# Optimization experiments

Hardware: AMD Instinct MI355X
Metric: run time of the kernel (lower is better)

Reference implementation:

```python
import jax, jax.numpy as jnp
import numpy as np

T = 65536  # number of frames

# Precomputed strict upper-triangle index pairs (matches htriu/ptriu/ltriu masks:
# dist+1 >= 1 > 0 everywhere, so boolean_mask((dist+1)*triu != 0) followed by -1
# is exactly 'take dist at strict upper-triangle entries').
_HIU = np.triu_indices(21, k=1)  # 210 pairs
_PIU = np.triu_indices(25, k=1)  # 300 pairs
_LIU = np.triu_indices(20, k=1)  # 190 pairs


def _triu_dist(pts, iu):
    # pts: (T, N, C); returns (T, P) pairwise Euclidean distances at i<j pairs
    d = pts[:, iu[0], :] - pts[:, iu[1], :]
    return jnp.sqrt(jnp.sum(d * d, axis=-1))


def setup_inputs() -> dict:
    key = jax.random.key(0)
    x = jax.random.normal(key, (T, 115, 3), dtype=jnp.float32)
    return {"x": x}


def reference(x):
    # NaN -> 0
    x = jnp.where(jnp.isnan(x), jnp.float32(0.0), x)
    lefth = x[:, 40:61, :]   # (T, 21, 3)
    righth = x[:, 94:115, :] # (T, 21, 3)
    pose = x[:, 61:86, :]    # (T, 25, 3)
    lip = x[:, :40, :]       # (T, 40, 3)

    # pick the dominant hand (global scalar condition)
    lefth_sum = jnp.sum((lefth != 0).astype(jnp.float32))
    righth_sum = jnp.sum((righth != 0).astype(jnp.float32))
    cond = lefth_sum > righth_sum

    h_x = jnp.where(cond, lefth, righth)  # (T, 21, 3)
    xfeat = jnp.where(cond,
                      jnp.concatenate([lefth, pose, lip], axis=1),
                      jnp.concatenate([righth, pose, lip], axis=1))  # (T, 86, 3)

    # mirror x-coordinate for left hand
    xc = jnp.where(cond, -xfeat[:, :, 0], xfeat[:, :, 0])
    xfeat = jnp.concatenate([xc[:, :, None], xfeat[:, :, 1:]], axis=-1)

    # frame compaction: drop frames whose hand is all-zero.
    # Implemented as a stable sort of the keep mask (kept frames first, order
    # preserved) so shapes stay static; with randn inputs every frame is kept
    # and this is exactly tf.boolean_mask.
    keep = jnp.sum(h_x.reshape(-1, 21 * 3), axis=1) != 0
    order = jnp.argsort(jnp.logical_not(keep), stable=True)
    xfeat = xfeat[order]

    # temporal deltas, zero-padded at the end
    dxyz = jnp.concatenate(
        [xfeat[:-1] - xfeat[1:], jnp.zeros((1, 86, 3), dtype=xfeat.dtype)], axis=0)

    hdist = _triu_dist(xfeat[:, :21, :3], _HIU)     # (T, 210) hand pairwise
    pdist = _triu_dist(xfeat[:, 21:46, :2], _PIU)   # (T, 300) pose pairwise (xy)
    oldist = _triu_dist(xfeat[:, 46:66, :2], _LIU)  # (T, 190) outer lip (xy)
    ildist = _triu_dist(xfeat[:, 66:86, :2], _LIU)  # (T, 190) inner lip (xy)

    out = jnp.concatenate([
        xfeat[:, :21, :3].reshape(-1, 21 * 3),
        xfeat[:, 21:46, :2].reshape(-1, 25 * 2),
        xfeat[:, 46:66, :2].reshape(-1, 20 * 2),
        dxyz[:, :21, :3].reshape(-1, 21 * 3),
        dxyz[:, 21:46, :2].reshape(-1, 25 * 2),
        dxyz[:, 46:66, :2].reshape(-1, 20 * 2),
        hdist, pdist, oldist, ildist,
    ], axis=-1)  # (T, 1196)

    out = out[:100]
    return out.reshape(1, -1, 1196)
```

## Files before the change

kernel.cpp:

```cpp
#include <hip/hip_runtime.h>
#include <math.h>

#define T_FRAMES 65536
#define FSTRIDE  345
#define ROWB     4784


__device__ __forceinline__ void triu_ab(int l, int N, int& a, int& b) {
  int a0 = 0, rem = l, row = N - 1;
  while (rem >= row) { rem -= row; ++a0; --row; }
  a = a0; b = a0 + 1 + rem;
}

__global__ __launch_bounds__(256) void phase1(const float* __restrict__ x,
                                              ushort* __restrict__ keepbits,
                                              int2* __restrict__ partials) {
  const int wave = threadIdx.x >> 6;
  const int lane = threadIdx.x & 63;
  const int w = (blockIdx.x << 2) + wave;
  const float* xw = x + (size_t)w * 8 * FSTRIDE;

  int cl = 0, cr = 0;
  unsigned bits = 0;
  for (int i = 0; i < 8; ++i) {
    const float* xf = xw + i * FSTRIDE;
    float a = 0.f, b = 0.f;
    if (lane < 63) {
      a = xf[120 + lane]; if (isnan(a)) a = 0.f;
      b = xf[282 + lane]; if (isnan(b)) b = 0.f;
    }
    cl += (a != 0.f);
    cr += (b != 0.f);
    float va = a, vb = b;
    for (int off = 32; off > 0; off >>= 1) {
      va += __shfl_down(va, off, 64);
      vb += __shfl_down(vb, off, 64);
    }
    if (lane == 0)
      bits |= (((va != 0.f) ? 1u : 0u) << (2 * i)) |
              (((vb != 0.f) ? 1u : 0u) << (2 * i + 1));
  }
  for (int off = 32; off > 0; off >>= 1) {
    cl += __shfl_down(cl, off, 64);
    cr += __shfl_down(cr, off, 64);
  }
  __shared__ int bL[4], bR[4];
  if (lane == 0) {
    keepbits[w] = (ushort)bits;
    bL[wave] = cl; bR[wave] = cr;
  }
  __syncthreads();
  if (threadIdx.x == 0)
    partials[blockIdx.x] = make_int2(bL[0] + bL[1] + bL[2] + bL[3],
                                     bR[0] + bR[1] + bR[2] + bR[3]);
}

__global__ __launch_bounds__(1024) void phase2(const uint4* __restrict__ kb,
                                               const int4* __restrict__ pp,
                                               char* __restrict__ outB) {
  const int tid  = threadIdx.x;
  const int lane = tid & 63;
  const int wave = tid >> 6;
  __shared__ unsigned int sKeep[4096];
  __shared__ int sL[16], sR[16];
  __shared__ unsigned long long sM[16];
  __shared__ int sOrder[104];
  __shared__ int sBase, sCond;

  uint4 v = kb[tid];
  sKeep[tid * 4 + 0] = v.x; sKeep[tid * 4 + 1] = v.y;
  sKeep[tid * 4 + 2] = v.z; sKeep[tid * 4 + 3] = v.w;

  int4 p = pp[tid];
  int cl = p.x + p.z, cr = p.y + p.w;
  for (int off = 32; off > 0; off >>= 1) {
    cl += __shfl_down(cl, off, 64);
    cr += __shfl_down(cr, off, 64);
  }
  if (lane == 0) { sL[wave] = cl; sR[wave] = cr; }
  __syncthreads();
  if (tid == 0) {
    int L = 0, R = 0;
    for (int i = 0; i < 16; ++i) { L += sL[i]; R += sR[i]; }
    sCond = (L > R) ? 1 : 0;
    sBase = 0;
  }
  __syncthreads();
  const int cond = sCond;
  const int sel  = cond ? 0 : 1;

  for (int pass = 0; pass < 2; ++pass) {
    for (int base = 0; base < T_FRAMES; base += 1024) {
      if (sBase >= 101) break;
      const int f = base + tid;
      const unsigned u = sKeep[f >> 4];
      int flag = (int)((u >> (((f >> 3) & 1) * 16 + (f & 7) * 2 + sel)) & 1u);
      if (pass) flag ^= 1;
      unsigned long long m = __ballot(flag);
      if (lane == 0) sM[wave] = m;
      __syncthreads();
      int pos = sBase;
      for (int w2 = 0; w2 < wave; ++w2) pos += (int)__popcll(sM[w2]);
      pos += (int)__popcll(m & ((1ull << lane) - 1ull));
      if (flag && pos < 101) sOrder[pos] = f;
      __syncthreads();
      if (tid == 0) {
        int tot = 0;
        for (int w2 = 0; w2 < 16; ++w2) tot += (int)__popcll(sM[w2]);
        sBase += tot;
      }
      __syncthreads();
    }
  }
  __syncthreads();
  if (tid < 100) {
    int4 rec;
    rec.x = cond; rec.y = sOrder[tid]; rec.z = sOrder[tid + 1]; rec.w = 0;
    *(int4*)(outB + (size_t)tid * ROWB) = rec;
  }
}

__global__ __launch_bounds__(256) void phase3(const float* __restrict__ x,
                                              float* __restrict__ out) {
  __shared__ float A[258], B[258];
  const int row = blockIdx.x;
  float* o = out + (size_t)row * 1196;
  const int4 rec = *(const int4*)o;
  const int cond = rec.x;
  const int f = rec.y, g = rec.z;
  const float* xf = x + (size_t)f * FSTRIDE;
  const float* xg = x + (size_t)g * FSTRIDE;

  for (int idx = threadIdx.x; idx < 258; idx += blockDim.x) {
    const int p = idx / 3, c = idx - p * 3;
    const int s = (p < 21) ? (cond ? 40 + p : 94 + p) : ((p < 46) ? p + 40 : p - 46);
    float va = xf[s * 3 + c]; if (isnan(va)) va = 0.f;
    float vb = xg[s * 3 + c]; if (isnan(vb)) vb = 0.f;
    if (cond && c == 0) { va = -va; vb = -vb; }
    A[idx] = va; B[idx] = vb;
  }
  __syncthreads();

  for (int j = threadIdx.x; j < 1196; j += blockDim.x) {
    float v;
    if (j < 306) {
      int jj = j; bool diff = false;
      if (jj >= 153) { diff = true; jj -= 153; }
      int p, c;
      if (jj < 63)       { p = jj / 3;             c = jj - p * 3; }
      else if (jj < 113) { int t = jj - 63;  p = 21 + (t >> 1); c = t & 1; }
      else               { int t = jj - 113; p = 46 + (t >> 1); c = t & 1; }
      v = A[p * 3 + c];
      if (diff) v -= B[p * 3 + c];
    } else if (j < 516) {
      int a, b; triu_ab(j - 306, 21, a, b);
      const float dx = A[a*3]   - A[b*3];
      const float dy = A[a*3+1] - A[b*3+1];
      const float dz = A[a*3+2] - A[b*3+2];
      v = sqrtf(dx*dx + dy*dy + dz*dz);
    } else if (j < 816) {
      int a, b; triu_ab(j - 516, 25, a, b);
      a += 21; b += 21;
      const float dx = A[a*3] - A[b*3], dy = A[a*3+1] - A[b*3+1];
      v = sqrtf(dx*dx + dy*dy);
    } else if (j < 1006) {
      int a, b; triu_ab(j - 816, 20, a, b);
      a += 46; b += 46;
      const float dx = A[a*3] - A[b*3], dy = A[a*3+1] - A[b*3+1];
      v = sqrtf(dx*dx + dy*dy);
    } else {
      int a, b; triu_ab(j - 1006, 20, a, b);
      a += 66; b += 66;
      const float dx = A[a*3] - A[b*3], dy = A[a*3+1] - A[b*3+1];
      v = sqrtf(dx*dx + dy*dy);
    }
    o[j] = v;
  }
}

extern "C" void kernel_launch(void* const* d_in, const int* in_sizes, int n_in,
                              void* d_out, int out_size, void* d_ws, size_t ws_size,
                              hipStream_t stream) {
  (void)in_sizes; (void)n_in; (void)out_size; (void)d_ws; (void)ws_size;
  const float* x = (const float*)d_in[0];
  char* ob = (char*)d_out;
  ushort* keepbits = (ushort*)ob;
  int2*   partials = (int2*)(ob + 16384);

  phase1<<<2048, 256, 0, stream>>>(x, keepbits, partials);
  phase2<<<1, 1024, 0, stream>>>((const uint4*)ob, (const int4*)(ob + 16384), ob);
  phase3<<<100, 256, 0, stream>>>(x, (float*)d_out);
}
```

Baseline: 134.6 us.

## Fuse compaction and feature kernels using per-block popcount rank selection

Merges the single-block serial compaction kernel into the per-row feature kernel. Each of the 100 blocks now rebuilds the dominant-hand decision and runs a popcount prefix scan over separate left and right keep bitmaps to find its own frame and the next frame. This removes one launch and the serial 1024-thread ballot loop, and moves the scratch buffers from the output to the workspace. In exchange every block repeats the reduction and the scan over 8 KB of bits.

```diff
diff --git a/kernel.cpp b/kernel.cpp
--- a/kernel.cpp
+++ b/kernel.cpp
@@ -3,7 +3,6 @@
 
 #define T_FRAMES 65536
 #define FSTRIDE  345
-#define ROWB     4784
 
 
 __device__ __forceinline__ void triu_ab(int l, int N, int& a, int& b) {
@@ -13,7 +12,8 @@
 }
 
 __global__ __launch_bounds__(256) void phase1(const float* __restrict__ x,
-                                              ushort* __restrict__ keepbits,
+                                              unsigned char* __restrict__ lbytes,
+                                              unsigned char* __restrict__ rbytes,
                                               int2* __restrict__ partials) {
   const int wave = threadIdx.x >> 6;
   const int lane = threadIdx.x & 63;
@@ -21,7 +21,7 @@
   const float* xw = x + (size_t)w * 8 * FSTRIDE;
 
   int cl = 0, cr = 0;
-  unsigned bits = 0;
+  unsigned lb = 0, rb = 0;
   for (int i = 0; i < 8; ++i) {
     const float* xf = xw + i * FSTRIDE;
     float a = 0.f, b = 0.f;
@@ -36,9 +36,10 @@
       va += __shfl_down(va, off, 64);
       vb += __shfl_down(vb, off, 64);
     }
-    if (lane == 0)
-      bits |= (((va != 0.f) ? 1u : 0u) << (2 * i)) |
-              (((vb != 0.f) ? 1u : 0u) << (2 * i + 1));
+    if (lane == 0) {
+      lb |= ((va != 0.f) ? 1u : 0u) << i;
+      rb |= ((vb != 0.f) ? 1u : 0u) << i;
+    }
   }
   for (int off = 32; off > 0; off >>= 1) {
     cl += __shfl_down(cl, off, 64);
@@ -46,7 +47,8 @@
   }
   __shared__ int bL[4], bR[4];
   if (lane == 0) {
-    keepbits[w] = (ushort)bits;
+    lbytes[w] = (unsigned char)lb;
+    rbytes[w] = (unsigned char)rb;
     bL[wave] = cl; bR[wave] = cr;
   }
   __syncthreads();
@@ -55,24 +57,24 @@
                                      bR[0] + bR[1] + bR[2] + bR[3]);
 }
 
-__global__ __launch_bounds__(1024) void phase2(const uint4* __restrict__ kb,
+__global__ __launch_bounds__(256) void phase23(const float* __restrict__ x,
+                                               const unsigned int* __restrict__ lbits,
+                                               const unsigned int* __restrict__ rbits,
                                                const int4* __restrict__ pp,
-                                               char* __restrict__ outB) {
+                                               float* __restrict__ out) {
   const int tid  = threadIdx.x;
   const int lane = tid & 63;
   const int wave = tid >> 6;
-  __shared__ unsigned int sKeep[4096];
-  __shared__ int sL[16], sR[16];
-  __shared__ unsigned long long sM[16];
-  __shared__ int sOrder[104];
-  __shared__ int sBase, sCond;
-
-  uint4 v = kb[tid];
-  sKeep[tid * 4 + 0] = v.x; sKeep[tid * 4 + 1] = v.y;
-  sKeep[tid * 4 + 2] = v.z; sKeep[tid * 4 + 3] = v.w;
-
-  int4 p = pp[tid];
-  int cl = p.x + p.z, cr = p.y + p.w;
+  const int row  = blockIdx.x;
+  __shared__ int sL[4], sR[4], sW[4];
+  __shared__ int sCond, sSel[2];
+  __shared__ float A[258], B[258];
+
+  int cl = 0, cr = 0;
+  for (int i = tid; i < 1024; i += 256) {
+    int4 p = pp[i];
+    cl += p.x + p.z; cr += p.y + p.w;
+  }
   for (int off = 32; off > 0; off >>= 1) {
     cl += __shfl_down(cl, off, 64);
     cr += __shfl_down(cr, off, 64);
@@ -80,58 +82,74 @@
   if (lane == 0) { sL[wave] = cl; sR[wave] = cr; }
   __syncthreads();
   if (tid == 0) {
-    int L = 0, R = 0;
-    for (int i = 0; i < 16; ++i) { L += sL[i]; R += sR[i]; }
+    int L = sL[0] + sL[1] + sL[2] + sL[3];
+    int R = sR[0] + sR[1] + sR[2] + sR[3];
     sCond = (L > R) ? 1 : 0;
-    sBase = 0;
   }
   __syncthreads();
   const int cond = sCond;
-  const int sel  = cond ? 0 : 1;
-
-  for (int pass = 0; pass < 2; ++pass) {
-    for (int base = 0; base < T_FRAMES; base += 1024) {
-      if (sBase >= 101) break;
-      const int f = base + tid;
-      const unsigned u = sKeep[f >> 4];
-      int flag = (int)((u >> (((f >> 3) & 1) * 16 + (f & 7) * 2 + sel)) & 1u);
-      if (pass) flag ^= 1;
-      unsigned long long m = __ballot(flag);
-      if (lane == 0) sM[wave] = m;
-      __syncthreads();
-      int pos = sBase;
-      for (int w2 = 0; w2 < wave; ++w2) pos += (int)__popcll(sM[w2]);
-      pos += (int)__popcll(m & ((1ull << lane) - 1ull));
-      if (flag && pos < 101) sOrder[pos] = f;
-      __syncthreads();
-      if (tid == 0) {
-        int tot = 0;
-        for (int w2 = 0; w2 < 16; ++w2) tot += (int)__popcll(sM[w2]);
-        sBase += tot;
+
+  const unsigned int* bits = cond ? lbits : rbits;
+  unsigned int wd[8];
+  int pc = 0;
+  #pragma unroll
+  for (int k = 0; k < 8; ++k) { wd[k] = bits[tid * 8 + k]; pc += __popc(wd[k]); }
+  int v = pc;
+  for (int off = 1; off < 64; off <<= 1) {
+    int u = __shfl_up(v, off, 64);
+    if (lane >= off) v += u;
+  }
+  if (lane == 63) sW[wave] = v;
+  __syncthreads();
+  int woff = 0;
+  for (int i = 0; i < wave; ++i) woff += sW[i];
+  const int Ktot = sW[0] + sW[1] + sW[2] + sW[3];
+  const int excl = woff + v - pc;
+
+  #pragma unroll
+  for (int j = 0; j < 2; ++j) {
+    const int r = row + 1 + j;
+    if (r <= Ktot) {
+      if (excl < r && r <= excl + pc) {
+        int rem = r - excl;
+        #pragma unroll
+        for (int k = 0; k < 8; ++k) {
+          const int c = __popc(wd[k]);
+          if (rem <= c) {
+            unsigned int ww = wd[k];
+            for (int q = 1; q < rem; ++q) ww &= ww - 1;
+            sSel[j] = (tid * 8 + k) * 32 + (__ffs(ww) - 1);
+            break;
+          }
+          rem -= c;
+        }
       }
-      __syncthreads();
-    }
-  }
-  __syncthreads();
-  if (tid < 100) {
-    int4 rec;
-    rec.x = cond; rec.y = sOrder[tid]; rec.z = sOrder[tid + 1]; rec.w = 0;
-    *(int4*)(outB + (size_t)tid * ROWB) = rec;
-  }
-}
-
-__global__ __launch_bounds__(256) void phase3(const float* __restrict__ x,
-                                              float* __restrict__ out) {
-  __shared__ float A[258], B[258];
-  const int row = blockIdx.x;
-  float* o = out + (size_t)row * 1196;
-  const int4 rec = *(const int4*)o;
-  const int cond = rec.x;
-  const int f = rec.y, g = rec.z;
+    } else {
+      const int rz = r - Ktot;
+      const int zexcl = 256 * tid - excl, zpc = 256 - pc;
+      if (zexcl < rz && rz <= zexcl + zpc) {
+        int rem = rz - zexcl;
+        #pragma unroll
+        for (int k = 0; k < 8; ++k) {
+          const unsigned int word = ~wd[k];
+          const int c = __popc(word);
+          if (rem <= c) {
+            unsigned int ww = word;
+            for (int q = 1; q < rem; ++q) ww &= ww - 1;
+            sSel[j] = (tid * 8 + k) * 32 + (__ffs(ww) - 1);
+            break;
+          }
+          rem -= c;
+        }
+      }
+    }
+  }
+  __syncthreads();
+  const int f = sSel[0], g = sSel[1];
   const float* xf = x + (size_t)f * FSTRIDE;
   const float* xg = x + (size_t)g * FSTRIDE;
 
-  for (int idx = threadIdx.x; idx < 258; idx += blockDim.x) {
+  for (int idx = tid; idx < 258; idx += 256) {
     const int p = idx / 3, c = idx - p * 3;
     const int s = (p < 21) ? (cond ? 40 + p : 94 + p) : ((p < 46) ? p + 40 : p - 46);
     float va = xf[s * 3 + c]; if (isnan(va)) va = 0.f;
@@ -141,8 +159,9 @@
   }
   __syncthreads();
 
-  for (int j = threadIdx.x; j < 1196; j += blockDim.x) {
-    float v;
+  float* o = out + (size_t)row * 1196;
+  for (int j = tid; j < 1196; j += 256) {
+    float val;
     if (j < 306) {
       int jj = j; bool diff = false;
       if (jj >= 153) { diff = true; jj -= 153; }
@@ -150,44 +169,46 @@
       if (jj < 63)       { p = jj / 3;             c = jj - p * 3; }
       else if (jj < 113) { int t = jj - 63;  p = 21 + (t >> 1); c = t & 1; }
       else               { int t = jj - 113; p = 46 + (t >> 1); c = t & 1; }
-      v = A[p * 3 + c];
-      if (diff) v -= B[p * 3 + c];
+      val = A[p * 3 + c];
+      if (diff) val -= B[p * 3 + c];
     } else if (j < 516) {
       int a, b; triu_ab(j - 306, 21, a, b);
       const float dx = A[a*3]   - A[b*3];
       const float dy = A[a*3+1] - A[b*3+1];
       const float dz = A[a*3+2] - A[b*3+2];
-      v = sqrtf(dx*dx + dy*dy + dz*dz);
+      val = sqrtf(dx*dx + dy*dy + dz*dz);
     } else if (j < 816) {
       int a, b; triu_ab(j - 516, 25, a, b);
       a += 21; b += 21;
       const float dx = A[a*3] - A[b*3], dy = A[a*3+1] - A[b*3+1];
-      v = sqrtf(dx*dx + dy*dy);
+      val = sqrtf(dx*dx + dy*dy);
     } else if (j < 1006) {
       int a, b; triu_ab(j - 816, 20, a, b);
       a += 46; b += 46;
       const float dx = A[a*3] - A[b*3], dy = A[a*3+1] - A[b*3+1];
-      v = sqrtf(dx*dx + dy*dy);
+      val = sqrtf(dx*dx + dy*dy);
     } else {
       int a, b; triu_ab(j - 1006, 20, a, b);
       a += 66; b += 66;
       const float dx = A[a*3] - A[b*3], dy = A[a*3+1] - A[b*3+1];
-      v = sqrtf(dx*dx + dy*dy);
-    }
-    o[j] = v;
+      val = sqrtf(dx*dx + dy*dy);
+    }
+    o[j] = val;
   }
 }
 
 extern "C" void kernel_launch(void* const* d_in, const int* in_sizes, int n_in,
                               void* d_out, int out_size, void* d_ws, size_t ws_size,
                               hipStream_t stream) {
-  (void)in_sizes; (void)n_in; (void)out_size; (void)d_ws; (void)ws_size;
+  (void)in_sizes; (void)n_in; (void)out_size; (void)ws_size;
   const float* x = (const float*)d_in[0];
-  char* ob = (char*)d_out;
-  ushort* keepbits = (ushort*)ob;
-  int2*   partials = (int2*)(ob + 16384);
-
-  phase1<<<2048, 256, 0, stream>>>(x, keepbits, partials);
-  phase2<<<1, 1024, 0, stream>>>((const uint4*)ob, (const int4*)(ob + 16384), ob);
-  phase3<<<100, 256, 0, stream>>>(x, (float*)d_out);
-}
+  char* ws = (char*)d_ws;
+  unsigned char* lbytes = (unsigned char*)ws;
+  unsigned char* rbytes = (unsigned char*)(ws + 8192);
+  int2*          partials = (int2*)(ws + 16384);
+
+  phase1<<<2048, 256, 0, stream>>>(x, lbytes, rbytes, partials);
+  phase23<<<100, 256, 0, stream>>>(x, (const unsigned int*)ws,
+                                   (const unsigned int*)(ws + 8192),
+                                   (const int4*)(ws + 16384), (float*)d_out);
+}
```

Result: no change. 135.0 us (+0.3%).
